# Performance work log

Measured on AMD Instinct MI355X. Metric: run time of the kernel, lower is better.

Reference implementation:

```python
import jax, jax.numpy as jnp
import numpy as np

B = 64                      # batch_size: number of candidate elements
N_PER = 100_000             # observations per candidate
DATA = B * N_PER            # data_size
EPS = 1e-6
INV_ROOT_2PI = 1.0 / np.sqrt(2.0 * np.pi)

def _deg2dist(deg):
    # chord distance on unit sphere subtended by angle deg
    return 2.0 * np.sin(np.radians(deg) / 2.0)

THRESH_DEG = 1.0
THRESH_S2_MIN = np.float32(_deg2dist(10.0 / 3600.0) ** 2)
THRESH_S2_MAX = np.float32(_deg2dist(THRESH_DEG) ** 2)
LOG_THRESH_S2_RANGE = np.float32(np.log(THRESH_S2_MAX / THRESH_S2_MIN))


def setup_inputs() -> dict:
    key = jax.random.key(0)
    k1, k2, k3, k4, k5 = jax.random.split(key, 5)
    u_obs = jax.random.normal(k1, (DATA, 3), dtype=jnp.float32)
    u_obs = u_obs / jnp.linalg.norm(u_obs, axis=-1, keepdims=True)   # unit directions
    # predicted directions = observed + small perturbation so some obs fall inside threshold
    u_pred = u_obs + 0.01 * jax.random.normal(k2, (DATA, 3), dtype=jnp.float32)
    u_pred = u_pred / jnp.linalg.norm(u_pred, axis=-1, keepdims=True)
    mag_obs = 18.0 + jax.random.normal(k3, (DATA,), dtype=jnp.float32)
    R_elt = 0.001 + 0.004 * jax.random.uniform(k4, (B,), dtype=jnp.float32)  # resolution param
    thresh_s2_ = jax.random.uniform(k5, (B,), dtype=jnp.float32)             # trainable, in [0,1]
    seg_ids = jnp.repeat(jnp.arange(B, dtype=jnp.int32), N_PER)              # ragged row_lengths -> segment ids
    return {"u_pred": u_pred, "R_elt": R_elt, "u_obs": u_obs,
            "mag_obs": mag_obs, "thresh_s2_": thresh_s2_, "seg_ids": seg_ids}


def reference(u_pred, R_elt, u_obs, mag_obs, thresh_s2_, seg_ids):
    # threshold transform (get_thresh_s2)
    thresh_s2_elt = THRESH_S2_MIN * jnp.exp(thresh_s2_ * LOG_THRESH_S2_RANGE)    # [B]
    thresh_all = thresh_s2_elt[seg_ids]                                          # [DATA]

    # calc_dist: squared chord distance + threshold mask
    du = u_pred - u_obs
    s2 = jnp.sum(du * du, axis=-1)                                               # [DATA]
    is_close = s2 < thresh_all                                                   # bool [DATA]
    mask = is_close.astype(s2.dtype)
    v = s2 / thresh_all                                                          # in [0,1] on close obs

    # cond_pdf_dist: exponential-family pdf conditional on a hit (q_miss = 1)
    lam_elt = 0.5 * thresh_s2_elt / (R_elt * R_elt)                              # [B]
    lam = lam_elt[seg_ids]                                                       # [DATA]
    log_q_hit = -lam * v + jnp.log(lam) - jnp.log1p(-jnp.exp(-lam))              # log(e^{-lam v} lam / (1 - e^{-lam}))

    # mag_standardize: per-candidate mean/std over close observations -> z-score
    n_close = jax.ops.segment_sum(mask, seg_ids, num_segments=B, indices_are_sorted=True)
    n_safe = jnp.maximum(n_close, 1.0)
    sum_m = jax.ops.segment_sum(mask * mag_obs, seg_ids, num_segments=B, indices_are_sorted=True)
    sum_m2 = jax.ops.segment_sum(mask * mag_obs * mag_obs, seg_ids, num_segments=B, indices_are_sorted=True)
    mu = sum_m / n_safe                                                          # [B]
    var = jnp.maximum(sum_m2 / n_safe - mu * mu, EPS)
    sigma_hat = jnp.sqrt(var)                                                    # [B]

    z = (mag_obs - mu[seg_ids]) / sigma_hat[seg_ids]                             # [DATA]
    log_p_mag = jnp.log(INV_ROOT_2PI / sigma_hat[seg_ids]) - 0.5 * z * z

    # per-candidate score: segment-sum of log conditional densities on close obs
    score = jax.ops.segment_sum(mask * (log_q_hit + log_p_mag), seg_ids,
                                num_segments=B, indices_are_sorted=True)         # [B]
    return score
```

## Files before the change

### kernel.cpp

```cpp
#include <hip/hip_runtime.h>
#include <math.h>


#define BLOCK 256
#define BPS   25

__global__ __launch_bounds__(BLOCK) void ts_main_kernel(
    const float* __restrict__ u_pred,
    const float* __restrict__ u_obs,
    const float* __restrict__ mag,
    const float* __restrict__ thresh_raw,
    float* __restrict__ acc,
    int n_per, float ts_min, float log_range)
{
    const int seg   = blockIdx.x / BPS;
    const int cid   = blockIdx.x % BPS;
    const int chunk = n_per / BPS;
    const long long base0 = (long long)seg * n_per + (long long)cid * chunk;

    const float thresh = ts_min * expf(thresh_raw[seg] * log_range);

    float cnt = 0.f, sm = 0.f, sm2 = 0.f, ss2 = 0.f;

    const int ngroups = chunk >> 2;
    for (int g = threadIdx.x; g < ngroups; g += BLOCK) {
        const long long base = base0 + ((long long)g << 2);
        const float4* up = reinterpret_cast<const float4*>(u_pred + base * 3);
        const float4* uo = reinterpret_cast<const float4*>(u_obs  + base * 3);
        const float4  a0 = up[0], a1 = up[1], a2 = up[2];
        const float4  b0 = uo[0], b1 = uo[1], b2 = uo[2];
        const float4  mg = *reinterpret_cast<const float4*>(mag + base);

        float dx, dy, dz, s2;

        dx = a0.x - b0.x; dy = a0.y - b0.y; dz = a0.z - b0.z;
        s2 = dx*dx + dy*dy + dz*dz;
        if (s2 < thresh) { cnt += 1.f; sm += mg.x; sm2 += mg.x*mg.x; ss2 += s2; }

        dx = a0.w - b0.w; dy = a1.x - b1.x; dz = a1.y - b1.y;
        s2 = dx*dx + dy*dy + dz*dz;
        if (s2 < thresh) { cnt += 1.f; sm += mg.y; sm2 += mg.y*mg.y; ss2 += s2; }

        dx = a1.z - b1.z; dy = a1.w - b1.w; dz = a2.x - b2.x;
        s2 = dx*dx + dy*dy + dz*dz;
        if (s2 < thresh) { cnt += 1.f; sm += mg.z; sm2 += mg.z*mg.z; ss2 += s2; }

        dx = a2.y - b2.y; dy = a2.z - b2.z; dz = a2.w - b2.w;
        s2 = dx*dx + dy*dy + dz*dz;
        if (s2 < thresh) { cnt += 1.f; sm += mg.w; sm2 += mg.w*mg.w; ss2 += s2; }
    }

    for (int off = 32; off > 0; off >>= 1) {
        cnt += __shfl_down(cnt, off);
        sm  += __shfl_down(sm,  off);
        sm2 += __shfl_down(sm2, off);
        ss2 += __shfl_down(ss2, off);
    }

    __shared__ float red[4][BLOCK / 64];
    const int wave = threadIdx.x >> 6;
    const int lane = threadIdx.x & 63;
    if (lane == 0) {
        red[0][wave] = cnt; red[1][wave] = sm;
        red[2][wave] = sm2; red[3][wave] = ss2;
    }
    __syncthreads();
    if (threadIdx.x == 0) {
        float t0 = 0.f, t1 = 0.f, t2 = 0.f, t3 = 0.f;
        #pragma unroll
        for (int w = 0; w < BLOCK / 64; ++w) {
            t0 += red[0][w]; t1 += red[1][w]; t2 += red[2][w]; t3 += red[3][w];
        }
        atomicAdd(&acc[seg * 4 + 0], t0);
        atomicAdd(&acc[seg * 4 + 1], t1);
        atomicAdd(&acc[seg * 4 + 2], t2);
        atomicAdd(&acc[seg * 4 + 3], t3);
    }
}

__global__ void ts_final_kernel(
    const float* __restrict__ acc,
    const float* __restrict__ R_elt,
    const float* __restrict__ thresh_raw,
    float* __restrict__ out,
    int Bn, float ts_min, float log_range)
{
    const int b = blockIdx.x * blockDim.x + threadIdx.x;
    if (b >= Bn) return;

    const float n   = acc[b * 4 + 0];
    const float sm  = acc[b * 4 + 1];
    const float sm2 = acc[b * 4 + 2];
    const float ss2 = acc[b * 4 + 3];

    float score = 0.f;
    if (n > 0.f) {
        const float thresh = ts_min * expf(thresh_raw[b] * log_range);
        const float R   = R_elt[b];
        const float lam = 0.5f * thresh / (R * R);
        const float C   = logf(lam) - logf(-expm1f(-lam));

        const float ssd     = sm2 - sm * (sm / n);
        const float var_raw = ssd / n;
        const float var     = fmaxf(var_raw, 1e-6f);
        const float sigma   = sqrtf(var);
        const float log_inv_root_2pi = -0.9189385332046727f;

        score = -lam * (ss2 / thresh)
              + n * C
              + n * (log_inv_root_2pi - logf(sigma))
              - 0.5f * (ssd / var);
    }
    out[b] = score;
}

extern "C" void kernel_launch(void* const* d_in, const int* in_sizes, int n_in,
                              void* d_out, int out_size, void* d_ws, size_t ws_size,
                              hipStream_t stream) {
    const float* u_pred     = (const float*)d_in[0];
    const float* R_elt      = (const float*)d_in[1];
    const float* u_obs      = (const float*)d_in[2];
    const float* mag_obs    = (const float*)d_in[3];
    const float* thresh_raw = (const float*)d_in[4];

    const int B    = in_sizes[1];
    const int DATA = in_sizes[3];
    const int n_per = DATA / B;

    float* acc = (float*)d_ws;
    float* out = (float*)d_out;

    const double rad_min = M_PI / 180.0 * (10.0 / 3600.0);
    const double rad_max = M_PI / 180.0 * 1.0;
    const float ts_min = (float)((2.0 * sin(rad_min / 2.0)) * (2.0 * sin(rad_min / 2.0)));
    const float ts_max = (float)((2.0 * sin(rad_max / 2.0)) * (2.0 * sin(rad_max / 2.0)));
    const float log_range = logf(ts_max / ts_min);

    hipMemsetAsync(acc, 0, (size_t)B * 4 * sizeof(float), stream);

    ts_main_kernel<<<B * BPS, BLOCK, 0, stream>>>(
        u_pred, u_obs, mag_obs, thresh_raw, acc, n_per, ts_min, log_range);

    ts_final_kernel<<<1, 64, 0, stream>>>(
        acc, R_elt, thresh_raw, out, B, ts_min, log_range);
}
```

Measured before the change: 42.92 us.

## Use many small single-pass blocks with conditional mag loads and skipped atomics

Replaces the 25-blocks-per-segment strided loop with a grid where each thread processes exactly two 4-observation groups (2048 observations per block), issuing all loads up front. The mag load is now performed only when at least one of a group's observations passes the threshold, and blocks with zero close observations skip their atomics. This raises memory-level parallelism and cuts mag traffic for sparse masks, at the cost of many more blocks and atomics per segment.

```diff
diff --git a/kernel.cpp b/kernel.cpp
--- a/kernel.cpp
+++ b/kernel.cpp
@@ -3,7 +3,7 @@
 
 
 #define BLOCK 256
-#define BPS   25
+#define OBS_PER_BLOCK (BLOCK * 8)
 
 __global__ __launch_bounds__(BLOCK) void ts_main_kernel(
     const float* __restrict__ u_pred,
@@ -11,43 +11,68 @@
     const float* __restrict__ mag,
     const float* __restrict__ thresh_raw,
     float* __restrict__ acc,
-    int n_per, float ts_min, float log_range)
+    int n_per, int bpseg, float ts_min, float log_range)
 {
-    const int seg   = blockIdx.x / BPS;
-    const int cid   = blockIdx.x % BPS;
-    const int chunk = n_per / BPS;
-    const long long base0 = (long long)seg * n_per + (long long)cid * chunk;
+    const int seg = blockIdx.x / bpseg;
+    const int cid = blockIdx.x - seg * bpseg;
+    const int tgroups = n_per >> 2;
+
+    int gA = cid * (2 * BLOCK) + threadIdx.x;
+    int gB = gA + BLOCK;
+    const bool vA = gA < tgroups;
+    const bool vB = gB < tgroups;
+    if (!vA) gA = 0;
+    if (!vB) gB = 0;
+
+    const long long segbase = (long long)seg * n_per;
+    const long long baseA = segbase + ((long long)gA << 2);
+    const long long baseB = segbase + ((long long)gB << 2);
 
     const float thresh = ts_min * expf(thresh_raw[seg] * log_range);
 
+    const float4* upA = reinterpret_cast<const float4*>(u_pred + baseA * 3);
+    const float4* uoA = reinterpret_cast<const float4*>(u_obs  + baseA * 3);
+    const float4* upB = reinterpret_cast<const float4*>(u_pred + baseB * 3);
+    const float4* uoB = reinterpret_cast<const float4*>(u_obs  + baseB * 3);
+    const float4 a0 = upA[0], a1 = upA[1], a2 = upA[2];
+    const float4 b0 = uoA[0], b1 = uoA[1], b2 = uoA[2];
+    const float4 c0 = upB[0], c1 = upB[1], c2 = upB[2];
+    const float4 d0 = uoB[0], d1 = uoB[1], d2 = uoB[2];
+
+    float s2A[4], s2B[4];
+    {
+        float dx, dy, dz;
+        dx = a0.x-b0.x; dy = a0.y-b0.y; dz = a0.z-b0.z; s2A[0] = dx*dx+dy*dy+dz*dz;
+        dx = a0.w-b0.w; dy = a1.x-b1.x; dz = a1.y-b1.y; s2A[1] = dx*dx+dy*dy+dz*dz;
+        dx = a1.z-b1.z; dy = a1.w-b1.w; dz = a2.x-b2.x; s2A[2] = dx*dx+dy*dy+dz*dz;
+        dx = a2.y-b2.y; dy = a2.z-b2.z; dz = a2.w-b2.w; s2A[3] = dx*dx+dy*dy+dz*dz;
+        dx = c0.x-d0.x; dy = c0.y-d0.y; dz = c0.z-d0.z; s2B[0] = dx*dx+dy*dy+dz*dz;
+        dx = c0.w-d0.w; dy = c1.x-d1.x; dz = c1.y-d1.y; s2B[1] = dx*dx+dy*dy+dz*dz;
+        dx = c1.z-d1.z; dy = c1.w-d1.w; dz = c2.x-d2.x; s2B[2] = dx*dx+dy*dy+dz*dz;
+        dx = c2.y-d2.y; dy = c2.z-d2.z; dz = c2.w-d2.w; s2B[3] = dx*dx+dy*dy+dz*dz;
+    }
+
+    bool clA[4], clB[4];
+    #pragma unroll
+    for (int i = 0; i < 4; ++i) { clA[i] = vA && (s2A[i] < thresh); }
+    #pragma unroll
+    for (int i = 0; i < 4; ++i) { clB[i] = vB && (s2B[i] < thresh); }
+
     float cnt = 0.f, sm = 0.f, sm2 = 0.f, ss2 = 0.f;
 
-    const int ngroups = chunk >> 2;
-    for (int g = threadIdx.x; g < ngroups; g += BLOCK) {
-        const long long base = base0 + ((long long)g << 2);
-        const float4* up = reinterpret_cast<const float4*>(u_pred + base * 3);
-        const float4* uo = reinterpret_cast<const float4*>(u_obs  + base * 3);
-        const float4  a0 = up[0], a1 = up[1], a2 = up[2];
-        const float4  b0 = uo[0], b1 = uo[1], b2 = uo[2];
-        const float4  mg = *reinterpret_cast<const float4*>(mag + base);
-
-        float dx, dy, dz, s2;
-
-        dx = a0.x - b0.x; dy = a0.y - b0.y; dz = a0.z - b0.z;
-        s2 = dx*dx + dy*dy + dz*dz;
-        if (s2 < thresh) { cnt += 1.f; sm += mg.x; sm2 += mg.x*mg.x; ss2 += s2; }
-
-        dx = a0.w - b0.w; dy = a1.x - b1.x; dz = a1.y - b1.y;
-        s2 = dx*dx + dy*dy + dz*dz;
-        if (s2 < thresh) { cnt += 1.f; sm += mg.y; sm2 += mg.y*mg.y; ss2 += s2; }
-
-        dx = a1.z - b1.z; dy = a1.w - b1.w; dz = a2.x - b2.x;
-        s2 = dx*dx + dy*dy + dz*dz;
-        if (s2 < thresh) { cnt += 1.f; sm += mg.z; sm2 += mg.z*mg.z; ss2 += s2; }
-
-        dx = a2.y - b2.y; dy = a2.z - b2.z; dz = a2.w - b2.w;
-        s2 = dx*dx + dy*dy + dz*dz;
-        if (s2 < thresh) { cnt += 1.f; sm += mg.w; sm2 += mg.w*mg.w; ss2 += s2; }
+    if (clA[0] | clA[1] | clA[2] | clA[3]) {
+        const float4 mg = *reinterpret_cast<const float4*>(mag + baseA);
+        const float m[4] = {mg.x, mg.y, mg.z, mg.w};
+        #pragma unroll
+        for (int i = 0; i < 4; ++i)
+            if (clA[i]) { cnt += 1.f; sm += m[i]; sm2 += m[i]*m[i]; ss2 += s2A[i]; }
+    }
+    if (clB[0] | clB[1] | clB[2] | clB[3]) {
+        const float4 mg = *reinterpret_cast<const float4*>(mag + baseB);
+        const float m[4] = {mg.x, mg.y, mg.z, mg.w};
+        #pragma unroll
+        for (int i = 0; i < 4; ++i)
+            if (clB[i]) { cnt += 1.f; sm += m[i]; sm2 += m[i]*m[i]; ss2 += s2B[i]; }
     }
 
     for (int off = 32; off > 0; off >>= 1) {
@@ -71,10 +96,12 @@
         for (int w = 0; w < BLOCK / 64; ++w) {
             t0 += red[0][w]; t1 += red[1][w]; t2 += red[2][w]; t3 += red[3][w];
         }
-        atomicAdd(&acc[seg * 4 + 0], t0);
-        atomicAdd(&acc[seg * 4 + 1], t1);
-        atomicAdd(&acc[seg * 4 + 2], t2);
-        atomicAdd(&acc[seg * 4 + 3], t3);
+        if (t0 != 0.f) {
+            atomicAdd(&acc[seg * 4 + 0], t0);
+            atomicAdd(&acc[seg * 4 + 1], t1);
+            atomicAdd(&acc[seg * 4 + 2], t2);
+            atomicAdd(&acc[seg * 4 + 3], t3);
+        }
     }
 }
 
@@ -123,8 +150,8 @@
     const float* mag_obs    = (const float*)d_in[3];
     const float* thresh_raw = (const float*)d_in[4];
 
-    const int B    = in_sizes[1];
-    const int DATA = in_sizes[3];
+    const int B     = in_sizes[1];
+    const int DATA  = in_sizes[3];
     const int n_per = DATA / B;
 
     float* acc = (float*)d_ws;
@@ -136,10 +163,12 @@
     const float ts_max = (float)((2.0 * sin(rad_max / 2.0)) * (2.0 * sin(rad_max / 2.0)));
     const float log_range = logf(ts_max / ts_min);
 
+    const int bpseg = (n_per + OBS_PER_BLOCK - 1) / OBS_PER_BLOCK;
+
     hipMemsetAsync(acc, 0, (size_t)B * 4 * sizeof(float), stream);
 
-    ts_main_kernel<<<B * BPS, BLOCK, 0, stream>>>(
-        u_pred, u_obs, mag_obs, thresh_raw, acc, n_per, ts_min, log_range);
+    ts_main_kernel<<<B * bpseg, BLOCK, 0, stream>>>(
+        u_pred, u_obs, mag_obs, thresh_raw, acc, n_per, bpseg, ts_min, log_range);
 
     ts_final_kernel<<<1, 64, 0, stream>>>(
         acc, R_elt, thresh_raw, out, B, ts_min, log_range);
```

After: 50.05 us. 16.6% more time.

## Double-buffer global-to-LDS async loads per wave with fewer blocks per segment

Applied to the files above, without the earlier changes.

Replaces direct per-thread float4 global loads with per-wave asynchronous global_load_lds transfers into a double-buffered LDS region, overlapping the next tile's fetch with compute on the current one. Cuts blocks per segment from 25 to 8, with each wave striding over 256-observation tiles, and skips atomics when a block found no close observations. Tail handling clamps addresses and masks invalid lanes. The fewer, larger blocks and hand-written waitcnt asm risk lower occupancy and ordering hazards in exchange for better memory-latency hiding.

```diff
diff --git a/kernel.cpp b/kernel.cpp
--- a/kernel.cpp
+++ b/kernel.cpp
@@ -3,7 +3,19 @@
 
 
 #define BLOCK 256
-#define BPS   25
+#define WAVES (BLOCK / 64)
+#define SEG_BLOCKS 8
+#define WAVES_PER_SEG (SEG_BLOCKS * WAVES)
+#define OBS_PER_ITER 256
+#define BUF_FLOATS 1792
+#define WAVE_LDS (2 * BUF_FLOATS)
+
+typedef const __attribute__((address_space(1))) unsigned int g_u32;
+typedef __attribute__((address_space(3))) unsigned int l_u32;
+
+__device__ __forceinline__ void ld_lds16(const float* g, float* l) {
+    __builtin_amdgcn_global_load_lds((g_u32*)g, (l_u32*)l, 16, 0, 0);
+}
 
 __global__ __launch_bounds__(BLOCK) void ts_main_kernel(
     const float* __restrict__ u_pred,
@@ -13,41 +25,89 @@
     float* __restrict__ acc,
     int n_per, float ts_min, float log_range)
 {
-    const int seg   = blockIdx.x / BPS;
-    const int cid   = blockIdx.x % BPS;
-    const int chunk = n_per / BPS;
-    const long long base0 = (long long)seg * n_per + (long long)cid * chunk;
+    __shared__ float lds[WAVES * WAVE_LDS];
+    __shared__ float red[4][WAVES];
+
+    const int seg  = blockIdx.x / SEG_BLOCKS;
+    const int cid  = blockIdx.x % SEG_BLOCKS;
+    const int widx = threadIdx.x >> 6;
+    const int lane = threadIdx.x & 63;
+    const int wv   = cid * WAVES + widx;
+
+    float* wlds = &lds[widx * WAVE_LDS];
+
+    const long long segO = (long long)seg * n_per;
+    const float* predBase = u_pred + segO * 3;
+    const float* obsBase  = u_obs  + segO * 3;
+    const float* magBase  = mag + segO;
+
+    const int  niter  = (n_per + OBS_PER_ITER - 1) / OBS_PER_ITER;
+    const long long dirMax = (long long)n_per * 3 - 4;
+    const long long magMax = (long long)n_per - 4;
 
     const float thresh = ts_min * expf(thresh_raw[seg] * log_range);
 
+    auto stage = [&](int buf, int it) {
+        float* b = wlds + buf * BUF_FLOATS;
+        const long long fbase = (long long)it * 768;
+        #pragma unroll
+        for (int c = 0; c < 3; ++c) {
+            long long fo = fbase + c * 256 + lane * 4;
+            if (fo > dirMax) fo = dirMax;
+            ld_lds16(predBase + fo, b + c * 256);
+        }
+        #pragma unroll
+        for (int c = 0; c < 3; ++c) {
+            long long fo = fbase + c * 256 + lane * 4;
+            if (fo > dirMax) fo = dirMax;
+            ld_lds16(obsBase + fo, b + 768 + c * 256);
+        }
+        long long mo = (long long)it * 256 + lane * 4;
+        if (mo > magMax) mo = magMax;
+        ld_lds16(magBase + mo, b + 1536);
+    };
+
     float cnt = 0.f, sm = 0.f, sm2 = 0.f, ss2 = 0.f;
 
-    const int ngroups = chunk >> 2;
-    for (int g = threadIdx.x; g < ngroups; g += BLOCK) {
-        const long long base = base0 + ((long long)g << 2);
-        const float4* up = reinterpret_cast<const float4*>(u_pred + base * 3);
-        const float4* uo = reinterpret_cast<const float4*>(u_obs  + base * 3);
-        const float4  a0 = up[0], a1 = up[1], a2 = up[2];
-        const float4  b0 = uo[0], b1 = uo[1], b2 = uo[2];
-        const float4  mg = *reinterpret_cast<const float4*>(mag + base);
-
-        float dx, dy, dz, s2;
-
-        dx = a0.x - b0.x; dy = a0.y - b0.y; dz = a0.z - b0.z;
-        s2 = dx*dx + dy*dy + dz*dz;
-        if (s2 < thresh) { cnt += 1.f; sm += mg.x; sm2 += mg.x*mg.x; ss2 += s2; }
-
-        dx = a0.w - b0.w; dy = a1.x - b1.x; dz = a1.y - b1.y;
-        s2 = dx*dx + dy*dy + dz*dz;
-        if (s2 < thresh) { cnt += 1.f; sm += mg.y; sm2 += mg.y*mg.y; ss2 += s2; }
-
-        dx = a1.z - b1.z; dy = a1.w - b1.w; dz = a2.x - b2.x;
-        s2 = dx*dx + dy*dy + dz*dz;
-        if (s2 < thresh) { cnt += 1.f; sm += mg.z; sm2 += mg.z*mg.z; ss2 += s2; }
-
-        dx = a2.y - b2.y; dy = a2.z - b2.z; dz = a2.w - b2.w;
-        s2 = dx*dx + dy*dy + dz*dz;
-        if (s2 < thresh) { cnt += 1.f; sm += mg.w; sm2 += mg.w*mg.w; ss2 += s2; }
+    int it = wv;
+    if (it < niter) stage(0, it);
+
+    int t = 0;
+    for (; it < niter; it += WAVES_PER_SEG, ++t) {
+        const int nxt = it + WAVES_PER_SEG;
+        const int cur = t & 1;
+        if (nxt < niter) {
+            stage(cur ^ 1, nxt);
+            asm volatile("s_waitcnt vmcnt(7)" ::: "memory");
+        } else {
+            asm volatile("s_waitcnt vmcnt(0)" ::: "memory");
+        }
+
+        const float* b = wlds + cur * BUF_FLOATS;
+        const float4 p0 = *reinterpret_cast<const float4*>(b + 12 * lane);
+        const float4 p1 = *reinterpret_cast<const float4*>(b + 12 * lane + 4);
+        const float4 p2 = *reinterpret_cast<const float4*>(b + 12 * lane + 8);
+        const float4 o0 = *reinterpret_cast<const float4*>(b + 768 + 12 * lane);
+        const float4 o1 = *reinterpret_cast<const float4*>(b + 768 + 12 * lane + 4);
+        const float4 o2 = *reinterpret_cast<const float4*>(b + 768 + 12 * lane + 8);
+        const float4 mg = *reinterpret_cast<const float4*>(b + 1536 + 4 * lane);
+
+        const bool valid = (it * OBS_PER_ITER + lane * 4) < n_per;
+
+        float s2[4];
+        {
+            float dx, dy, dz;
+            dx = p0.x-o0.x; dy = p0.y-o0.y; dz = p0.z-o0.z; s2[0] = dx*dx+dy*dy+dz*dz;
+            dx = p0.w-o0.w; dy = p1.x-o1.x; dz = p1.y-o1.y; s2[1] = dx*dx+dy*dy+dz*dz;
+            dx = p1.z-o1.z; dy = p1.w-o1.w; dz = p2.x-o2.x; s2[2] = dx*dx+dy*dy+dz*dz;
+            dx = p2.y-o2.y; dy = p2.z-o2.z; dz = p2.w-o2.w; s2[3] = dx*dx+dy*dy+dz*dz;
+        }
+        const float m[4] = {mg.x, mg.y, mg.z, mg.w};
+        #pragma unroll
+        for (int i = 0; i < 4; ++i) {
+            const bool cl = valid && (s2[i] < thresh);
+            if (cl) { cnt += 1.f; sm += m[i]; sm2 += m[i]*m[i]; ss2 += s2[i]; }
+        }
     }
 
     for (int off = 32; off > 0; off >>= 1) {
@@ -57,24 +117,23 @@
         ss2 += __shfl_down(ss2, off);
     }
 
-    __shared__ float red[4][BLOCK / 64];
-    const int wave = threadIdx.x >> 6;
-    const int lane = threadIdx.x & 63;
     if (lane == 0) {
-        red[0][wave] = cnt; red[1][wave] = sm;
-        red[2][wave] = sm2; red[3][wave] = ss2;
+        red[0][widx] = cnt; red[1][widx] = sm;
+        red[2][widx] = sm2; red[3][widx] = ss2;
     }
     __syncthreads();
     if (threadIdx.x == 0) {
         float t0 = 0.f, t1 = 0.f, t2 = 0.f, t3 = 0.f;
         #pragma unroll
-        for (int w = 0; w < BLOCK / 64; ++w) {
+        for (int w = 0; w < WAVES; ++w) {
             t0 += red[0][w]; t1 += red[1][w]; t2 += red[2][w]; t3 += red[3][w];
         }
-        atomicAdd(&acc[seg * 4 + 0], t0);
-        atomicAdd(&acc[seg * 4 + 1], t1);
-        atomicAdd(&acc[seg * 4 + 2], t2);
-        atomicAdd(&acc[seg * 4 + 3], t3);
+        if (t0 != 0.f) {
+            atomicAdd(&acc[seg * 4 + 0], t0);
+            atomicAdd(&acc[seg * 4 + 1], t1);
+            atomicAdd(&acc[seg * 4 + 2], t2);
+            atomicAdd(&acc[seg * 4 + 3], t3);
+        }
     }
 }
 
@@ -123,8 +182,8 @@
     const float* mag_obs    = (const float*)d_in[3];
     const float* thresh_raw = (const float*)d_in[4];
 
-    const int B    = in_sizes[1];
-    const int DATA = in_sizes[3];
+    const int B     = in_sizes[1];
+    const int DATA  = in_sizes[3];
     const int n_per = DATA / B;
 
     float* acc = (float*)d_ws;
@@ -138,7 +197,7 @@
 
     hipMemsetAsync(acc, 0, (size_t)B * 4 * sizeof(float), stream);
 
-    ts_main_kernel<<<B * BPS, BLOCK, 0, stream>>>(
+    ts_main_kernel<<<B * SEG_BLOCKS, BLOCK, 0, stream>>>(
         u_pred, u_obs, mag_obs, thresh_raw, acc, n_per, ts_min, log_range);
 
     ts_final_kernel<<<1, 64, 0, stream>>>(
```

After: 38.84 us, median of 2. 9.5% less time.

## Coalesce xyz loads per wave with strided float4 tiles and lane shuffles

Applied to the files above, without the earlier changes.

Each wave now processes 256-observation tiles. Every lane loads float4s at strides of 256 floats, so a wave's loads are fully coalesced instead of each thread reading 48 contiguous bytes. Squared component differences are reassembled into per-observation distances using shuffles from neighbouring lanes. Magnitudes are then read only for observations inside the threshold, which skips most of the mag traffic because few observations qualify. The change also uses 32 blocks per segment with occupancy hint 8 and skips atomics when a block has no hits, at the cost of more index arithmetic and divergent branches.

```diff
diff --git a/kernel.cpp b/kernel.cpp
--- a/kernel.cpp
+++ b/kernel.cpp
@@ -3,9 +3,13 @@
 
 
 #define BLOCK 256
-#define BPS   25
-
-__global__ __launch_bounds__(BLOCK) void ts_main_kernel(
+#define WAVES 4
+#define SEG_BLOCKS 32
+#define WPS (SEG_BLOCKS * WAVES)
+#define TILE_OBS 256
+#define TILE_FLT 768
+
+__global__ __launch_bounds__(BLOCK, 8) void ts_main_kernel(
     const float* __restrict__ u_pred,
     const float* __restrict__ u_obs,
     const float* __restrict__ mag,
@@ -13,41 +17,94 @@
     float* __restrict__ acc,
     int n_per, float ts_min, float log_range)
 {
-    const int seg   = blockIdx.x / BPS;
-    const int cid   = blockIdx.x % BPS;
-    const int chunk = n_per / BPS;
-    const long long base0 = (long long)seg * n_per + (long long)cid * chunk;
+    const int seg  = blockIdx.x / SEG_BLOCKS;
+    const int cid  = blockIdx.x % SEG_BLOCKS;
+    const int widx = threadIdx.x >> 6;
+    const int lane = threadIdx.x & 63;
+    const int wv   = cid * WAVES + widx;
+
+    const long long segO = (long long)seg * n_per;
+    const float* predB = u_pred + segO * 3;
+    const float* obsB  = u_obs  + segO * 3;
+    const float* magB  = mag + segO;
 
     const float thresh = ts_min * expf(thresh_raw[seg] * log_range);
 
+    const int nt    = (n_per + TILE_OBS - 1) / TILE_OBS;
+    const int lastT = nt - 1;
+    const int maxFo = n_per * 3 - 4;
+
     float cnt = 0.f, sm = 0.f, sm2 = 0.f, ss2 = 0.f;
 
-    const int ngroups = chunk >> 2;
-    for (int g = threadIdx.x; g < ngroups; g += BLOCK) {
-        const long long base = base0 + ((long long)g << 2);
-        const float4* up = reinterpret_cast<const float4*>(u_pred + base * 3);
-        const float4* uo = reinterpret_cast<const float4*>(u_obs  + base * 3);
-        const float4  a0 = up[0], a1 = up[1], a2 = up[2];
-        const float4  b0 = uo[0], b1 = uo[1], b2 = uo[2];
-        const float4  mg = *reinterpret_cast<const float4*>(mag + base);
-
-        float dx, dy, dz, s2;
-
-        dx = a0.x - b0.x; dy = a0.y - b0.y; dz = a0.z - b0.z;
-        s2 = dx*dx + dy*dy + dz*dz;
-        if (s2 < thresh) { cnt += 1.f; sm += mg.x; sm2 += mg.x*mg.x; ss2 += s2; }
-
-        dx = a0.w - b0.w; dy = a1.x - b1.x; dz = a1.y - b1.y;
-        s2 = dx*dx + dy*dy + dz*dz;
-        if (s2 < thresh) { cnt += 1.f; sm += mg.y; sm2 += mg.y*mg.y; ss2 += s2; }
-
-        dx = a1.z - b1.z; dy = a1.w - b1.w; dz = a2.x - b2.x;
-        s2 = dx*dx + dy*dy + dz*dz;
-        if (s2 < thresh) { cnt += 1.f; sm += mg.z; sm2 += mg.z*mg.z; ss2 += s2; }
-
-        dx = a2.y - b2.y; dy = a2.z - b2.z; dz = a2.w - b2.w;
-        s2 = dx*dx + dy*dy + dz*dz;
-        if (s2 < thresh) { cnt += 1.f; sm += mg.w; sm2 += mg.w*mg.w; ss2 += s2; }
+    for (int t = wv; t < nt; t += WPS) {
+        const int fbase = t * TILE_FLT + lane * 4;
+        float4 p0, p1, p2, o0, o1, o2;
+        if (t != lastT) {
+            const float* pp = predB + fbase;
+            const float* oo = obsB  + fbase;
+            p0 = *(const float4*)(pp);
+            p1 = *(const float4*)(pp + 256);
+            p2 = *(const float4*)(pp + 512);
+            o0 = *(const float4*)(oo);
+            o1 = *(const float4*)(oo + 256);
+            o2 = *(const float4*)(oo + 512);
+        } else {
+            const int f0 = min(fbase,       maxFo);
+            const int f1 = min(fbase + 256, maxFo);
+            const int f2 = min(fbase + 512, maxFo);
+            p0 = *(const float4*)(predB + f0);
+            p1 = *(const float4*)(predB + f1);
+            p2 = *(const float4*)(predB + f2);
+            o0 = *(const float4*)(obsB + f0);
+            o1 = *(const float4*)(obsB + f1);
+            o2 = *(const float4*)(obsB + f2);
+        }
+
+        float4 q0, q1, q2;
+        { float d;
+          d = p0.x-o0.x; q0.x = d*d;  d = p0.y-o0.y; q0.y = d*d;
+          d = p0.z-o0.z; q0.z = d*d;  d = p0.w-o0.w; q0.w = d*d;
+          d = p1.x-o1.x; q1.x = d*d;  d = p1.y-o1.y; q1.y = d*d;
+          d = p1.z-o1.z; q1.z = d*d;  d = p1.w-o1.w; q1.w = d*d;
+          d = p2.x-o2.x; q2.x = d*d;  d = p2.y-o2.y; q2.y = d*d;
+          d = p2.z-o2.z; q2.z = d*d;  d = p2.w-o2.w; q2.w = d*d; }
+
+        float nb00 = __shfl_down(q0.x, 1), nb01 = __shfl_down(q0.y, 1);
+        float nb10 = __shfl_down(q1.x, 1), nb11 = __shfl_down(q1.y, 1);
+        float nb20 = __shfl_down(q2.x, 1), nb21 = __shfl_down(q2.y, 1);
+        const float b10 = __shfl(q1.x, 0), b11 = __shfl(q1.y, 0);
+        const float b20 = __shfl(q2.x, 0);
+        if (lane == 63) { nb00 = b10; nb01 = b11; nb10 = b20; }
+
+        const int tbase = t * TILE_OBS;
+
+        auto doChunk = [&](int c, float a0, float a1, float a2, float a3,
+                           float nb0, float nb1) {
+            const int base = 256 * c + 4 * lane;
+            const int k0   = (3 - ((c + lane) % 3)) % 3;
+            const float u  = a1 + a2;
+            const float c0 = u + a0;
+            const float c1 = u + a3;
+            const float v  = a3 + nb0;
+            const float c2 = a2 + v;
+            const float c3 = v + nb1;
+            const float s2f = (k0 == 0) ? c0 : ((k0 == 1) ? c1 : c2);
+            const int jf = tbase + (base + k0) / 3;
+            if (jf < n_per && s2f < thresh) {
+                const float m = magB[jf];
+                cnt += 1.f; sm += m; sm2 += m * m; ss2 += s2f;
+            }
+            if (k0 == 0) {
+                const int js = jf + 1;
+                if (js < n_per && c3 < thresh) {
+                    const float m = magB[js];
+                    cnt += 1.f; sm += m; sm2 += m * m; ss2 += c3;
+                }
+            }
+        };
+        doChunk(0, q0.x, q0.y, q0.z, q0.w, nb00, nb01);
+        doChunk(1, q1.x, q1.y, q1.z, q1.w, nb10, nb11);
+        doChunk(2, q2.x, q2.y, q2.z, q2.w, nb20, nb21);
     }
 
     for (int off = 32; off > 0; off >>= 1) {
@@ -57,24 +114,24 @@
         ss2 += __shfl_down(ss2, off);
     }
 
-    __shared__ float red[4][BLOCK / 64];
-    const int wave = threadIdx.x >> 6;
-    const int lane = threadIdx.x & 63;
+    __shared__ float red[4][WAVES];
     if (lane == 0) {
-        red[0][wave] = cnt; red[1][wave] = sm;
-        red[2][wave] = sm2; red[3][wave] = ss2;
+        red[0][widx] = cnt; red[1][widx] = sm;
+        red[2][widx] = sm2; red[3][widx] = ss2;
     }
     __syncthreads();
     if (threadIdx.x == 0) {
         float t0 = 0.f, t1 = 0.f, t2 = 0.f, t3 = 0.f;
         #pragma unroll
-        for (int w = 0; w < BLOCK / 64; ++w) {
+        for (int w = 0; w < WAVES; ++w) {
             t0 += red[0][w]; t1 += red[1][w]; t2 += red[2][w]; t3 += red[3][w];
         }
-        atomicAdd(&acc[seg * 4 + 0], t0);
-        atomicAdd(&acc[seg * 4 + 1], t1);
-        atomicAdd(&acc[seg * 4 + 2], t2);
-        atomicAdd(&acc[seg * 4 + 3], t3);
+        if (t0 != 0.f) {
+            atomicAdd(&acc[seg * 4 + 0], t0);
+            atomicAdd(&acc[seg * 4 + 1], t1);
+            atomicAdd(&acc[seg * 4 + 2], t2);
+            atomicAdd(&acc[seg * 4 + 3], t3);
+        }
     }
 }
 
@@ -123,8 +180,8 @@
     const float* mag_obs    = (const float*)d_in[3];
     const float* thresh_raw = (const float*)d_in[4];
 
-    const int B    = in_sizes[1];
-    const int DATA = in_sizes[3];
+    const int B     = in_sizes[1];
+    const int DATA  = in_sizes[3];
     const int n_per = DATA / B;
 
     float* acc = (float*)d_ws;
@@ -138,7 +195,7 @@
 
     hipMemsetAsync(acc, 0, (size_t)B * 4 * sizeof(float), stream);
 
-    ts_main_kernel<<<B * BPS, BLOCK, 0, stream>>>(
+    ts_main_kernel<<<B * SEG_BLOCKS, BLOCK, 0, stream>>>(
         u_pred, u_obs, mag_obs, thresh_raw, acc, n_per, ts_min, log_range);
 
     ts_final_kernel<<<1, 64, 0, stream>>>(
```

Measured after the change: 51.46 us. 1.2x slower.
